# Kernel tuning notes

Hardware: AMD Instinct MI355X
Metric: run time of the kernel (lower is better)

## Reference

```python
import jax, jax.numpy as jnp
import numpy as np

NNZ = 20_000_000
DIM = 16384  # conceptual dense shape is (DIM, DIM)


def setup_inputs() -> dict:
    key = jax.random.key(0)
    kv, ki = jax.random.split(key)
    values = jax.random.normal(kv, (NNZ,), dtype=jnp.float32)
    indices = jax.random.randint(ki, (2, NNZ), 0, DIM, dtype=jnp.int64)
    return {"values": values, "indices": indices}


def reference(values, indices):
    # torch.sparse.sum(x) with no dim reduces every stored nonzero to a scalar.
    # Duplicate indices contribute additively, so this equals values.sum()
    # whether or not the COO tensor is coalesced. indices are not needed for
    # the full reduction but define the sparse structure.
    return jnp.sum(values)
```

## Files before the change

### kernel.cpp

```cpp
#include <hip/hip_runtime.h>


__global__ __launch_bounds__(256) void sum_reduce_kernel(
        const float* __restrict__ values, float* __restrict__ out, int n4) {
    const float4* __restrict__ v4 = reinterpret_cast<const float4*>(values);
    float s = 0.0f;
    const int stride = gridDim.x * blockDim.x;
    for (int i = blockIdx.x * blockDim.x + threadIdx.x; i < n4; i += stride) {
        float4 x = v4[i];
        s += (x.x + x.y) + (x.z + x.w);
    }
    #pragma unroll
    for (int off = 32; off > 0; off >>= 1)
        s += __shfl_down(s, off, 64);
    __shared__ float wsum[4];
    const int lane = threadIdx.x & 63;
    const int wave = threadIdx.x >> 6;
    if (lane == 0) wsum[wave] = s;
    __syncthreads();
    if (threadIdx.x == 0) {
        float t = (wsum[0] + wsum[1]) + (wsum[2] + wsum[3]);
        atomicAdd(out, t);
    }
}

extern "C" void kernel_launch(void* const* d_in, const int* in_sizes, int n_in,
                              void* d_out, int out_size, void* d_ws, size_t ws_size,
                              hipStream_t stream) {
    const float* values = (const float*)d_in[0];
    float* out = (float*)d_out;
    const int n = in_sizes[0];
    const int n4 = n / 4;

    sum_reduce_kernel<<<2048, 256, 0, stream>>>(values, out, n4);
}
```

Baseline: 249.2 us.

## Replace global atomicAdd with cooperative grid sync and single-block final reduction

New measurement: 354.4 us. 1.42x slower.

```diff
diff --git a/kernel.cpp b/kernel.cpp
--- a/kernel.cpp
+++ b/kernel.cpp
@@ -1,8 +1,12 @@
 #include <hip/hip_runtime.h>
+#include <hip/hip_cooperative_groups.h>
+
+namespace cg = cooperative_groups;
 
 
-__global__ __launch_bounds__(256) void sum_reduce_kernel(
-        const float* __restrict__ values, float* __restrict__ out, int n4) {
+__global__ __launch_bounds__(256) void fused_sum_kernel(
+        const float* __restrict__ values, float* __restrict__ out,
+        float* __restrict__ partials, int n4) {
     const float4* __restrict__ v4 = reinterpret_cast<const float4*>(values);
     float s = 0.0f;
     const int stride = gridDim.x * blockDim.x;
@@ -20,7 +24,24 @@
     __syncthreads();
     if (threadIdx.x == 0) {
         float t = (wsum[0] + wsum[1]) + (wsum[2] + wsum[3]);
-        atomicAdd(out, t);
+        __hip_atomic_store(&partials[blockIdx.x], t,
+                           __ATOMIC_RELAXED, __HIP_MEMORY_SCOPE_AGENT);
+    }
+    cg::this_grid().sync();
+    if (blockIdx.x == 0) {
+        float r = 0.0f;
+        const int nb = gridDim.x;
+        for (int i = threadIdx.x; i < nb; i += 256)
+            r += __hip_atomic_load(&partials[i],
+                                   __ATOMIC_RELAXED, __HIP_MEMORY_SCOPE_AGENT);
+        #pragma unroll
+        for (int off = 32; off > 0; off >>= 1)
+            r += __shfl_down(r, off, 64);
+        __shared__ float fsum[4];
+        if ((threadIdx.x & 63) == 0) fsum[threadIdx.x >> 6] = r;
+        __syncthreads();
+        if (threadIdx.x == 0)
+            out[0] = (fsum[0] + fsum[1]) + (fsum[2] + fsum[3]);
     }
 }
 
@@ -29,8 +50,12 @@
                               hipStream_t stream) {
     const float* values = (const float*)d_in[0];
     float* out = (float*)d_out;
+    float* partials = (float*)d_ws;
     const int n = in_sizes[0];
-    const int n4 = n / 4;
+    int n4 = n / 4;
 
-    sum_reduce_kernel<<<2048, 256, 0, stream>>>(values, out, n4);
+    dim3 grid(1024), block(256);
+    void* args[] = {(void*)&values, (void*)&out, (void*)&partials, (void*)&n4};
+    hipLaunchCooperativeKernel((const void*)fused_sum_kernel, grid, block,
+                               args, 0, stream);
 }
```
